# Kernel optimization log

Hardware: AMD Instinct MI355X
Metric: run time of the kernel (lower is better)

## Reference

```python
import jax, jax.numpy as jnp
import numpy as np

N = 50000          # num nodes
E = 800000         # num edges
IN_C = 128         # in_channels
OUT_C = 32         # out_channels
HEADS = 4
R = 8              # num_relations
HC = HEADS * OUT_C # 128
NEG_SLOPE = 0.2


def setup_inputs() -> dict:
    key = jax.random.key(0)
    k1, k2, k3, k4, k5, k6 = jax.random.split(key, 6)
    x = jax.random.normal(k1, (N, IN_C), dtype=jnp.float32)
    edge_index = jax.random.randint(k2, (2, E), 0, N, dtype=jnp.int64)
    edge_type = jax.random.randint(k3, (E,), 0, R, dtype=jnp.int64)
    # glorot init for params
    def glorot(k, shape, fan):
        lim = jnp.sqrt(6.0 / fan)
        return jax.random.uniform(k, shape, jnp.float32, -lim, lim)
    weight = glorot(k4, (R, IN_C, HC), IN_C + HC)       # [R, in, H*C]
    q = glorot(k5, (HC, HEADS), HC + HEADS)             # [H*C, H*dim], dim=1
    kk = glorot(k6, (HC, HEADS), HC + HEADS)
    bias = jnp.zeros((HC,), dtype=jnp.float32)
    return {"x": x, "edge_index": edge_index, "edge_type": edge_type,
            "weight": weight, "q": q, "k": kk, "bias": bias}


def reference(x, edge_index, edge_type, weight, q, k, bias):
    src, dst = edge_index[0], edge_index[1]  # x_j = x[src], x_i = x[dst]
    # Relation-specific transform: precompute per-node per-relation transform
    # (equivalent math to per-edge bmm with index_select'd weights).
    T = jnp.einsum('ni,rio->nro', x, weight)        # [N, R, HC]
    outi = T[dst, edge_type]                        # [E, HC]
    outj = T[src, edge_type]                        # [E, HC]
    qi = outi @ q                                   # [E, H]
    kj = outj @ k                                   # [E, H]
    alpha = jax.nn.leaky_relu(qi + kj, NEG_SLOPE)   # additive-self-attention
    # across-relation softmax over incoming edges of each target node
    amax = jax.ops.segment_max(alpha, dst, num_segments=N)       # [N, H]
    amax = jnp.where(jnp.isfinite(amax), amax, 0.0)
    ex = jnp.exp(alpha - amax[dst])
    denom = jax.ops.segment_sum(ex, dst, num_segments=N)         # [N, H]
    alpha = ex / (denom[dst] + 1e-16)               # [E, H]
    # message (mod=None, dropout=0): outj * alpha, then scatter-add aggregate
    msg = outj.reshape(E, HEADS, OUT_C) * alpha[:, :, None]      # [E, H, C]
    out = jax.ops.segment_sum(msg, dst, num_segments=N)          # [N, H, C]
    return out.reshape(N, HC) + bias                # concat=True
```

## Files before the change

### kernel.cpp

```cpp
#include <hip/hip_runtime.h>

#define NN 50000
#define EE 800000
#define INC 128
#define HCC 128
#define RR 8
#define HH 4
#define CHUNK 256

typedef __attribute__((ext_vector_type(8))) short bf16x8;
typedef __attribute__((ext_vector_type(4))) float f32x4;

static __device__ __forceinline__ unsigned f2b_rne(float f) {
    unsigned u = __float_as_uint(f);
    return (u + 0x7FFFu + ((u >> 16) & 1u)) >> 16;
}
static __device__ __forceinline__ float b2f(unsigned short s) {
    return __uint_as_float(((unsigned)s) << 16);
}


__global__ __launch_bounds__(256) void k_cvt_x(const float* __restrict__ x,
                                               unsigned short* __restrict__ xb) {
    int t = blockIdx.x * 256 + threadIdx.x;
    const float4* p = (const float4*)x + t * 2;
    float4 v0 = p[0], v1 = p[1];
    uint4 pk;
    pk.x = f2b_rne(v0.x) | (f2b_rne(v0.y) << 16);
    pk.y = f2b_rne(v0.z) | (f2b_rne(v0.w) << 16);
    pk.z = f2b_rne(v1.x) | (f2b_rne(v1.y) << 16);
    pk.w = f2b_rne(v1.z) | (f2b_rne(v1.w) << 16);
    *((uint4*)xb + t) = pk;
}

__global__ __launch_bounds__(256) void k_cvt_wt(const float* __restrict__ W,
                                                unsigned short* __restrict__ Wt) {
    int t = blockIdx.x * 256 + threadIdx.x;
    int m = t & 127, kb = (t >> 7) & 15, r = t >> 11;
    unsigned short tmp[8];
#pragma unroll
    for (int j = 0; j < 8; ++j)
        tmp[j] = (unsigned short)f2b_rne(W[((r << 7) + (kb << 3) + j) * 128 + m]);
    uint4 pk;
    pk.x = tmp[0] | ((unsigned)tmp[1] << 16);
    pk.y = tmp[2] | ((unsigned)tmp[3] << 16);
    pk.z = tmp[4] | ((unsigned)tmp[5] << 16);
    pk.w = tmp[6] | ((unsigned)tmp[7] << 16);
    *(uint4*)(Wt + ((r << 7) + m) * 128 + (kb << 3)) = pk;
}

__global__ __launch_bounds__(128) void k_wqk(const float* __restrict__ W,
                                             const float* __restrict__ qw,
                                             const float* __restrict__ kw,
                                             unsigned short* __restrict__ Wqkt) {
    int r = blockIdx.x, i = threadIdx.x;
    const float* wrow = W + (r * INC + i) * HCC;
    float aq0 = 0, aq1 = 0, aq2 = 0, aq3 = 0;
    float ak0 = 0, ak1 = 0, ak2 = 0, ak3 = 0;
    for (int o = 0; o < HCC; ++o) {
        float w = wrow[o];
        float4 qv = *(const float4*)(qw + o * 4);
        float4 kv = *(const float4*)(kw + o * 4);
        aq0 = fmaf(w, qv.x, aq0); aq1 = fmaf(w, qv.y, aq1);
        aq2 = fmaf(w, qv.z, aq2); aq3 = fmaf(w, qv.w, aq3);
        ak0 = fmaf(w, kv.x, ak0); ak1 = fmaf(w, kv.y, ak1);
        ak2 = fmaf(w, kv.z, ak2); ak3 = fmaf(w, kv.w, ak3);
    }
    int cq = r * 4, ck = 32 + r * 4;
    Wqkt[(cq + 0) * 128 + i] = (unsigned short)f2b_rne(aq0);
    Wqkt[(cq + 1) * 128 + i] = (unsigned short)f2b_rne(aq1);
    Wqkt[(cq + 2) * 128 + i] = (unsigned short)f2b_rne(aq2);
    Wqkt[(cq + 3) * 128 + i] = (unsigned short)f2b_rne(aq3);
    Wqkt[(ck + 0) * 128 + i] = (unsigned short)f2b_rne(ak0);
    Wqkt[(ck + 1) * 128 + i] = (unsigned short)f2b_rne(ak1);
    Wqkt[(ck + 2) * 128 + i] = (unsigned short)f2b_rne(ak2);
    Wqkt[(ck + 3) * 128 + i] = (unsigned short)f2b_rne(ak3);
}

__global__ __launch_bounds__(256, 4) void k_qk(const unsigned short* __restrict__ xb,
                                               const unsigned short* __restrict__ Wqkt,
                                               float* __restrict__ QT,
                                               float* __restrict__ KT) {
    int wave = (blockIdx.x * 256 + threadIdx.x) >> 6;
    int lane = threadIdx.x & 63;
    int nt0 = wave * 2, nt1 = nt0 + 1;
    if (nt0 >= 3125) return;
    bool has1 = nt1 < 3125;
    int ln = lane & 15, kq = lane >> 4;

    const unsigned short* x0 = xb + (nt0 * 16 + ln) * 128 + kq * 8;
    const unsigned short* x1 = xb + ((has1 ? nt1 : nt0) * 16 + ln) * 128 + kq * 8;
    bf16x8 b0[4], b1[4];
#pragma unroll
    for (int ks = 0; ks < 4; ++ks) {
        b0[ks] = *(const bf16x8*)(x0 + ks * 32);
        b1[ks] = *(const bf16x8*)(x1 + ks * 32);
    }
    const unsigned short* ab = Wqkt + ln * 128 + kq * 8;
#pragma unroll
    for (int mg = 0; mg < 4; ++mg) {
        f32x4 acc0 = {0.f, 0.f, 0.f, 0.f};
        f32x4 acc1 = {0.f, 0.f, 0.f, 0.f};
#pragma unroll
        for (int ks = 0; ks < 4; ++ks) {
            bf16x8 a = *(const bf16x8*)(ab + mg * 2048 + ks * 32);
            acc0 = __builtin_amdgcn_mfma_f32_16x16x32_bf16(a, b0[ks], acc0, 0, 0, 0);
            acc1 = __builtin_amdgcn_mfma_f32_16x16x32_bf16(a, b1[ks], acc1, 0, 0, 0);
        }
        float* base = (mg < 2) ? QT : KT;
        int rr = (mg & 1) * 4 + kq;
        *(f32x4*)(base + ((nt0 * 16 + ln) * 8 + rr) * 4) = acc0;
        if (has1) *(f32x4*)(base + ((nt1 * 16 + ln) * 8 + rr) * 4) = acc1;
    }
}

__global__ __launch_bounds__(256, 4) void k_T(const unsigned short* __restrict__ xb,
                                              const unsigned short* __restrict__ Wt,
                                              unsigned short* __restrict__ T) {
    int wave = (blockIdx.x * 256 + threadIdx.x) >> 6;
    int lane = threadIdx.x & 63;
    int r = wave & 7;
    int p = wave >> 3;
    int nt0 = p * 2, nt1 = nt0 + 1;
    bool has1 = nt1 < 3125;
    int ln = lane & 15, kq = lane >> 4;

    const unsigned short* x0 = xb + (nt0 * 16 + ln) * 128 + kq * 8;
    const unsigned short* x1 = xb + ((has1 ? nt1 : nt0) * 16 + ln) * 128 + kq * 8;
    bf16x8 b0[4], b1[4];
#pragma unroll
    for (int ks = 0; ks < 4; ++ks) {
        b0[ks] = *(const bf16x8*)(x0 + ks * 32);
        b1[ks] = *(const bf16x8*)(x1 + ks * 32);
    }
    const unsigned short* wb = Wt + (r * 128 + ln) * 128 + kq * 8;
#pragma unroll
    for (int mg2 = 0; mg2 < 4; ++mg2) {
        f32x4 e0 = {0.f, 0.f, 0.f, 0.f};
        f32x4 o0 = {0.f, 0.f, 0.f, 0.f};
        f32x4 e1 = {0.f, 0.f, 0.f, 0.f};
        f32x4 o1 = {0.f, 0.f, 0.f, 0.f};
#pragma unroll
        for (int ks = 0; ks < 4; ++ks) {
            bf16x8 ae = *(const bf16x8*)(wb + (2 * mg2) * 2048 + ks * 32);
            bf16x8 ao = *(const bf16x8*)(wb + (2 * mg2 + 1) * 2048 + ks * 32);
            e0 = __builtin_amdgcn_mfma_f32_16x16x32_bf16(ae, b0[ks], e0, 0, 0, 0);
            o0 = __builtin_amdgcn_mfma_f32_16x16x32_bf16(ao, b0[ks], o0, 0, 0, 0);
            e1 = __builtin_amdgcn_mfma_f32_16x16x32_bf16(ae, b1[ks], e1, 0, 0, 0);
            o1 = __builtin_amdgcn_mfma_f32_16x16x32_bf16(ao, b1[ks], o1, 0, 0, 0);
        }
        uint4 pk0, pk1;
        pk0.x = f2b_rne(e0[0]) | (f2b_rne(e0[1]) << 16);
        pk0.y = f2b_rne(e0[2]) | (f2b_rne(e0[3]) << 16);
        pk0.z = f2b_rne(o0[0]) | (f2b_rne(o0[1]) << 16);
        pk0.w = f2b_rne(o0[2]) | (f2b_rne(o0[3]) << 16);
        pk1.x = f2b_rne(e1[0]) | (f2b_rne(e1[1]) << 16);
        pk1.y = f2b_rne(e1[2]) | (f2b_rne(e1[3]) << 16);
        pk1.z = f2b_rne(o1[0]) | (f2b_rne(o1[1]) << 16);
        pk1.w = f2b_rne(o1[2]) | (f2b_rne(o1[3]) << 16);
        int pos = mg2 * 32 + kq * 8;
        *(uint4*)(T + ((nt0 * 16 + ln) * 8 + r) * 128 + pos) = pk0;
        if (has1) *(uint4*)(T + ((nt1 * 16 + ln) * 8 + r) * 128 + pos) = pk1;
    }
}

__global__ __launch_bounds__(256) void k_hist(const int* __restrict__ ei,
                                              int* __restrict__ deg) {
    int e = blockIdx.x * 256 + threadIdx.x;
    if (e >= EE) return;
    atomicAdd(&deg[ei[EE + e]], 1);
}

__global__ __launch_bounds__(1024) void k_scan1(const int* __restrict__ deg,
                                                int* __restrict__ rowptr,
                                                int* __restrict__ bsum) {
    __shared__ int s[1024];
    int tid = threadIdx.x;
    int g = blockIdx.x * 1024 + tid;
    int v = (g < NN) ? deg[g] : 0;
    s[tid] = v;
    __syncthreads();
    for (int off = 1; off < 1024; off <<= 1) {
        int t = (tid >= off) ? s[tid - off] : 0;
        __syncthreads();
        s[tid] += t;
        __syncthreads();
    }
    if (g < NN) rowptr[g + 1] = s[tid];
    if (tid == 1023) bsum[blockIdx.x] = s[1023];
}

__global__ void k_scan2(const int* __restrict__ bsum, int* __restrict__ boff) {
    int tid = threadIdx.x;
    const int NB = (NN + 1023) / 1024;
    int v = (tid < NB) ? bsum[tid] : 0;
    int orig = v;
    for (int off = 1; off < 64; off <<= 1) {
        int t = __shfl_up(v, off);
        if (tid >= off) v += t;
    }
    if (tid < NB) boff[tid] = v - orig;
}

__global__ __launch_bounds__(1024) void k_scan3(int* __restrict__ rowptr,
                                                const int* __restrict__ boff) {
    int tid = threadIdx.x;
    int g = blockIdx.x * 1024 + tid;
    if (g == 0) rowptr[0] = 0;
    if (g < NN) rowptr[g + 1] += boff[blockIdx.x];
}

__global__ __launch_bounds__(256) void k_scatter(const int* __restrict__ ei,
                                                 const int* __restrict__ et,
                                                 const int* __restrict__ rowptr,
                                                 int* __restrict__ cursor,
                                                 unsigned* __restrict__ srow) {
    int e = blockIdx.x * 256 + threadIdx.x;
    if (e >= EE) return;
    int src = ei[e], dst = ei[EE + e], r = et[e];
    int pos = rowptr[dst] + atomicAdd(&cursor[dst], 1);
    srow[pos] = (unsigned)(src * RR + r);
}

__global__ __launch_bounds__(64) void k_attagg(const int* __restrict__ rowptr,
                                               const unsigned* __restrict__ srow,
                                               const float* __restrict__ QT,
                                               const float* __restrict__ KT,
                                               const unsigned short* __restrict__ T,
                                               const float* __restrict__ bias,
                                               float* __restrict__ out) {
    __shared__ float als[CHUNK * 4];
    __shared__ unsigned srw[CHUNK];
    __shared__ float qs[32];
    const int n = blockIdx.x;
    const int lane = threadIdx.x;
    const int h = lane >> 4;
    const int c = lane * 2;
    const int mgv = c >> 4, kqv = (c >> 2) & 3, regv = c & 3;
    const int posu = (mgv >> 1) * 32 + kqv * 8 + (mgv & 1) * 4 + regv;
    const int beg = rowptr[n], end = rowptr[n + 1];

    if (lane < 32) qs[lane] = QT[n * 32 + lane];
    __syncthreads();

    float m0 = -3.0e38f, m1 = -3.0e38f, m2 = -3.0e38f, m3 = -3.0e38f;
    float d0 = 0.f, d1 = 0.f, d2 = 0.f, d3 = 0.f;
    float accx = 0.f, accy = 0.f;

    for (int j0 = beg; j0 < end; j0 += CHUNK) {
        const int cnt = min(CHUNK, end - j0);
        float lm0 = -3.0e38f, lm1 = -3.0e38f, lm2 = -3.0e38f, lm3 = -3.0e38f;
        for (int jj = lane; jj < cnt; jj += 64) {
            unsigned sr = srow[j0 + jj];
            srw[jj] = sr;
            int r = sr & 7;
            float4 kj = *(const float4*)(KT + sr * 4);
            float a0 = qs[r * 4 + 0] + kj.x;
            float a1 = qs[r * 4 + 1] + kj.y;
            float a2 = qs[r * 4 + 2] + kj.z;
            float a3 = qs[r * 4 + 3] + kj.w;
            a0 = a0 > 0.f ? a0 : 0.2f * a0;
            a1 = a1 > 0.f ? a1 : 0.2f * a1;
            a2 = a2 > 0.f ? a2 : 0.2f * a2;
            a3 = a3 > 0.f ? a3 : 0.2f * a3;
            als[jj * 4 + 0] = a0; als[jj * 4 + 1] = a1;
            als[jj * 4 + 2] = a2; als[jj * 4 + 3] = a3;
            lm0 = fmaxf(lm0, a0); lm1 = fmaxf(lm1, a1);
            lm2 = fmaxf(lm2, a2); lm3 = fmaxf(lm3, a3);
        }
        __syncthreads();
#pragma unroll
        for (int off = 1; off < 64; off <<= 1) {
            lm0 = fmaxf(lm0, __shfl_xor(lm0, off));
            lm1 = fmaxf(lm1, __shfl_xor(lm1, off));
            lm2 = fmaxf(lm2, __shfl_xor(lm2, off));
            lm3 = fmaxf(lm3, __shfl_xor(lm3, off));
        }
        float nm0 = fmaxf(m0, lm0), nm1 = fmaxf(m1, lm1);
        float nm2 = fmaxf(m2, lm2), nm3 = fmaxf(m3, lm3);
        float s0 = expf(m0 - nm0), s1 = expf(m1 - nm1);
        float s2 = expf(m2 - nm2), s3 = expf(m3 - nm3);
        d0 *= s0; d1 *= s1; d2 *= s2; d3 *= s3;
        float sh = h == 0 ? s0 : h == 1 ? s1 : h == 2 ? s2 : s3;
        accx *= sh; accy *= sh;
        m0 = nm0; m1 = nm1; m2 = nm2; m3 = nm3;
        float p0 = 0.f, p1 = 0.f, p2 = 0.f, p3 = 0.f;
        for (int jj = lane; jj < cnt; jj += 64) {
            float e0 = expf(als[jj * 4 + 0] - m0);
            float e1 = expf(als[jj * 4 + 1] - m1);
            float e2 = expf(als[jj * 4 + 2] - m2);
            float e3 = expf(als[jj * 4 + 3] - m3);
            als[jj * 4 + 0] = e0; als[jj * 4 + 1] = e1;
            als[jj * 4 + 2] = e2; als[jj * 4 + 3] = e3;
            p0 += e0; p1 += e1; p2 += e2; p3 += e3;
        }
#pragma unroll
        for (int off = 1; off < 64; off <<= 1) {
            p0 += __shfl_xor(p0, off);
            p1 += __shfl_xor(p1, off);
            p2 += __shfl_xor(p2, off);
            p3 += __shfl_xor(p3, off);
        }
        d0 += p0; d1 += p1; d2 += p2; d3 += p3;
        __syncthreads();
        for (int jj = 0; jj < cnt; ++jj) {
            float w = als[jj * 4 + h];
            unsigned pk = *(const unsigned*)(T + srw[jj] * 128 + posu);
            accx = fmaf(w, b2f((unsigned short)(pk & 0xFFFF)), accx);
            accy = fmaf(w, b2f((unsigned short)(pk >> 16)), accy);
        }
        __syncthreads();
    }
    float dh = h == 0 ? d0 : h == 1 ? d1 : h == 2 ? d2 : d3;
    float inv = 1.f / (dh + 1e-16f);
    out[n * 128 + c] = accx * inv + bias[c];
    out[n * 128 + c + 1] = accy * inv + bias[c + 1];
}

extern "C" void kernel_launch(void* const* d_in, const int* in_sizes, int n_in,
                              void* d_out, int out_size, void* d_ws, size_t ws_size,
                              hipStream_t stream) {
    const float* x    = (const float*)d_in[0];
    const int*   ei   = (const int*)d_in[1];
    const int*   et   = (const int*)d_in[2];
    const float* W    = (const float*)d_in[3];
    const float* qw   = (const float*)d_in[4];
    const float* kw   = (const float*)d_in[5];
    const float* bias = (const float*)d_in[6];
    float* out = (float*)d_out;
    char* ws = (char*)d_ws;

    unsigned short* T    = (unsigned short*)(ws + 0);
    float* QT            = (float*)(ws + 102400000);
    float* KT            = (float*)(ws + 108800000);
    unsigned short* Wqkt = (unsigned short*)(ws + 115200000);
    int* deg             = (int*)(ws + 115220480);
    int* cursor          = (int*)(ws + 115420480);
    int* rowptr          = (int*)(ws + 115620480);
    int* bsum            = (int*)(ws + 115820484);
    int* boff            = (int*)(ws + 115820740);
    unsigned* srow       = (unsigned*)(ws + 115820996);
    unsigned short* xb   = (unsigned short*)(ws + 119021056);
    unsigned short* Wt   = (unsigned short*)(ws + 131821056);

    hipMemsetAsync(ws + 115220480, 0, 400000, stream);

    k_cvt_x<<<3125, 256, 0, stream>>>(x, xb);
    k_cvt_wt<<<64, 256, 0, stream>>>(W, Wt);
    k_wqk<<<RR, 128, 0, stream>>>(W, qw, kw, Wqkt);
    k_qk<<<391, 256, 0, stream>>>(xb, Wqkt, QT, KT);
    k_T<<<3126, 256, 0, stream>>>(xb, Wt, T);
    k_hist<<<(EE + 255) / 256, 256, 0, stream>>>(ei, deg);
    k_scan1<<<49, 1024, 0, stream>>>(deg, rowptr, bsum);
    k_scan2<<<1, 64, 0, stream>>>(bsum, boff);
    k_scan3<<<49, 1024, 0, stream>>>(rowptr, boff);
    k_scatter<<<(EE + 255) / 256, 256, 0, stream>>>(ei, et, rowptr, cursor, srow);
    k_attagg<<<NN, 64, 0, stream>>>(rowptr, srow, QT, KT, T, bias, out);
}
```

Baseline: 311.3 us.

## Stage per-relation weights in XOR-swizzled LDS for the node-transform GEMM

Each k_T block now loads one relation's 128x128 bf16 weight tile into shared memory, stored in an XOR-swizzled layout that k_cvt_wt writes, and then computes 16 node tiles against it. The MFMA A operands are read from LDS instead of from global memory once per wave. This cuts global/L2 weight traffic and spreads LDS reads across banks. In exchange it needs a 32KB LDS allocation and a block barrier, drops the occupancy hint, and launches fewer, larger blocks.

```diff
diff --git a/kernel.cpp b/kernel.cpp
--- a/kernel.cpp
+++ b/kernel.cpp
@@ -34,7 +34,7 @@
 }
 
 __global__ __launch_bounds__(256) void k_cvt_wt(const float* __restrict__ W,
-                                                unsigned short* __restrict__ Wt) {
+                                                unsigned short* __restrict__ Wts) {
     int t = blockIdx.x * 256 + threadIdx.x;
     int m = t & 127, kb = (t >> 7) & 15, r = t >> 11;
     unsigned short tmp[8];
@@ -46,7 +46,8 @@
     pk.y = tmp[2] | ((unsigned)tmp[3] << 16);
     pk.z = tmp[4] | ((unsigned)tmp[5] << 16);
     pk.w = tmp[6] | ((unsigned)tmp[7] << 16);
-    *(uint4*)(Wt + ((r << 7) + m) * 128 + (kb << 3)) = pk;
+    int idx = r * 2048 + m * 16 + (kb ^ (m & 15));
+    *((uint4*)Wts + idx) = pk;
 }
 
 __global__ __launch_bounds__(128) void k_wqk(const float* __restrict__ W,
@@ -114,53 +115,69 @@
     }
 }
 
-__global__ __launch_bounds__(256, 4) void k_T(const unsigned short* __restrict__ xb,
-                                              const unsigned short* __restrict__ Wt,
-                                              unsigned short* __restrict__ T) {
-    int wave = (blockIdx.x * 256 + threadIdx.x) >> 6;
-    int lane = threadIdx.x & 63;
-    int r = wave & 7;
-    int p = wave >> 3;
-    int nt0 = p * 2, nt1 = nt0 + 1;
-    bool has1 = nt1 < 3125;
-    int ln = lane & 15, kq = lane >> 4;
-
-    const unsigned short* x0 = xb + (nt0 * 16 + ln) * 128 + kq * 8;
-    const unsigned short* x1 = xb + ((has1 ? nt1 : nt0) * 16 + ln) * 128 + kq * 8;
-    bf16x8 b0[4], b1[4];
-#pragma unroll
-    for (int ks = 0; ks < 4; ++ks) {
-        b0[ks] = *(const bf16x8*)(x0 + ks * 32);
-        b1[ks] = *(const bf16x8*)(x1 + ks * 32);
-    }
-    const unsigned short* wb = Wt + (r * 128 + ln) * 128 + kq * 8;
-#pragma unroll
-    for (int mg2 = 0; mg2 < 4; ++mg2) {
-        f32x4 e0 = {0.f, 0.f, 0.f, 0.f};
-        f32x4 o0 = {0.f, 0.f, 0.f, 0.f};
-        f32x4 e1 = {0.f, 0.f, 0.f, 0.f};
-        f32x4 o1 = {0.f, 0.f, 0.f, 0.f};
+__global__ __launch_bounds__(256) void k_T(const unsigned short* __restrict__ xb,
+                                           const unsigned short* __restrict__ Wts,
+                                           unsigned short* __restrict__ T) {
+    __shared__ unsigned short lA[16384];
+    const int r = blockIdx.x & 7;
+    const int grp = blockIdx.x >> 3;
+    const int tid = threadIdx.x;
+    const int wv = tid >> 6, lane = tid & 63;
+    const int ln = lane & 15, kq = lane >> 4;
+
+    {
+        const uint4* src = (const uint4*)Wts + r * 2048;
+        uint4* dst = (uint4*)lA;
+#pragma unroll
+        for (int i = 0; i < 8; ++i) dst[i * 256 + tid] = src[i * 256 + tid];
+    }
+    __syncthreads();
+
+#pragma unroll
+    for (int g = 0; g < 2; ++g) {
+        int nt0 = grp * 16 + g * 8 + wv * 2;
+        int nt1 = nt0 + 1;
+        bool h0 = nt0 < 3125, h1 = nt1 < 3125;
+        int a0 = h0 ? nt0 : 3124, a1 = h1 ? nt1 : 3124;
+        const unsigned short* x0 = xb + (a0 * 16 + ln) * 128 + kq * 8;
+        const unsigned short* x1 = xb + (a1 * 16 + ln) * 128 + kq * 8;
+        bf16x8 b0[4], b1[4];
 #pragma unroll
         for (int ks = 0; ks < 4; ++ks) {
-            bf16x8 ae = *(const bf16x8*)(wb + (2 * mg2) * 2048 + ks * 32);
-            bf16x8 ao = *(const bf16x8*)(wb + (2 * mg2 + 1) * 2048 + ks * 32);
-            e0 = __builtin_amdgcn_mfma_f32_16x16x32_bf16(ae, b0[ks], e0, 0, 0, 0);
-            o0 = __builtin_amdgcn_mfma_f32_16x16x32_bf16(ao, b0[ks], o0, 0, 0, 0);
-            e1 = __builtin_amdgcn_mfma_f32_16x16x32_bf16(ae, b1[ks], e1, 0, 0, 0);
-            o1 = __builtin_amdgcn_mfma_f32_16x16x32_bf16(ao, b1[ks], o1, 0, 0, 0);
-        }
-        uint4 pk0, pk1;
-        pk0.x = f2b_rne(e0[0]) | (f2b_rne(e0[1]) << 16);
-        pk0.y = f2b_rne(e0[2]) | (f2b_rne(e0[3]) << 16);
-        pk0.z = f2b_rne(o0[0]) | (f2b_rne(o0[1]) << 16);
-        pk0.w = f2b_rne(o0[2]) | (f2b_rne(o0[3]) << 16);
-        pk1.x = f2b_rne(e1[0]) | (f2b_rne(e1[1]) << 16);
-        pk1.y = f2b_rne(e1[2]) | (f2b_rne(e1[3]) << 16);
-        pk1.z = f2b_rne(o1[0]) | (f2b_rne(o1[1]) << 16);
-        pk1.w = f2b_rne(o1[2]) | (f2b_rne(o1[3]) << 16);
-        int pos = mg2 * 32 + kq * 8;
-        *(uint4*)(T + ((nt0 * 16 + ln) * 8 + r) * 128 + pos) = pk0;
-        if (has1) *(uint4*)(T + ((nt1 * 16 + ln) * 8 + r) * 128 + pos) = pk1;
+            b0[ks] = *(const bf16x8*)(x0 + ks * 32);
+            b1[ks] = *(const bf16x8*)(x1 + ks * 32);
+        }
+#pragma unroll
+        for (int mg2 = 0; mg2 < 4; ++mg2) {
+            f32x4 e0 = {0.f, 0.f, 0.f, 0.f};
+            f32x4 o0 = {0.f, 0.f, 0.f, 0.f};
+            f32x4 e1 = {0.f, 0.f, 0.f, 0.f};
+            f32x4 o1 = {0.f, 0.f, 0.f, 0.f};
+            const int rowe = mg2 * 32 + ln;
+            const int rowo = mg2 * 32 + 16 + ln;
+#pragma unroll
+            for (int ks = 0; ks < 4; ++ks) {
+                int ch = (kq + ks * 4) ^ ln;
+                bf16x8 ae = *(const bf16x8*)(lA + rowe * 128 + ch * 8);
+                bf16x8 ao = *(const bf16x8*)(lA + rowo * 128 + ch * 8);
+                e0 = __builtin_amdgcn_mfma_f32_16x16x32_bf16(ae, b0[ks], e0, 0, 0, 0);
+                o0 = __builtin_amdgcn_mfma_f32_16x16x32_bf16(ao, b0[ks], o0, 0, 0, 0);
+                e1 = __builtin_amdgcn_mfma_f32_16x16x32_bf16(ae, b1[ks], e1, 0, 0, 0);
+                o1 = __builtin_amdgcn_mfma_f32_16x16x32_bf16(ao, b1[ks], o1, 0, 0, 0);
+            }
+            uint4 pk0, pk1;
+            pk0.x = f2b_rne(e0[0]) | (f2b_rne(e0[1]) << 16);
+            pk0.y = f2b_rne(e0[2]) | (f2b_rne(e0[3]) << 16);
+            pk0.z = f2b_rne(o0[0]) | (f2b_rne(o0[1]) << 16);
+            pk0.w = f2b_rne(o0[2]) | (f2b_rne(o0[3]) << 16);
+            pk1.x = f2b_rne(e1[0]) | (f2b_rne(e1[1]) << 16);
+            pk1.y = f2b_rne(e1[2]) | (f2b_rne(e1[3]) << 16);
+            pk1.z = f2b_rne(o1[0]) | (f2b_rne(o1[1]) << 16);
+            pk1.w = f2b_rne(o1[2]) | (f2b_rne(o1[3]) << 16);
+            int pos = mg2 * 32 + kq * 8;
+            if (h0) *(uint4*)(T + ((nt0 * 16 + ln) * 8 + r) * 128 + pos) = pk0;
+            if (h1) *(uint4*)(T + ((nt1 * 16 + ln) * 8 + r) * 128 + pos) = pk1;
+        }
     }
 }
 
@@ -341,15 +358,15 @@
     int* boff            = (int*)(ws + 115820740);
     unsigned* srow       = (unsigned*)(ws + 115820996);
     unsigned short* xb   = (unsigned short*)(ws + 119021056);
-    unsigned short* Wt   = (unsigned short*)(ws + 131821056);
+    unsigned short* Wts  = (unsigned short*)(ws + 131821056);
 
     hipMemsetAsync(ws + 115220480, 0, 400000, stream);
 
     k_cvt_x<<<3125, 256, 0, stream>>>(x, xb);
-    k_cvt_wt<<<64, 256, 0, stream>>>(W, Wt);
+    k_cvt_wt<<<64, 256, 0, stream>>>(W, Wts);
     k_wqk<<<RR, 128, 0, stream>>>(W, qw, kw, Wqkt);
     k_qk<<<391, 256, 0, stream>>>(xb, Wqkt, QT, KT);
-    k_T<<<3126, 256, 0, stream>>>(xb, Wt, T);
+    k_T<<<8 * 196, 256, 0, stream>>>(xb, Wts, T);
     k_hist<<<(EE + 255) / 256, 256, 0, stream>>>(ei, deg);
     k_scan1<<<49, 1024, 0, stream>>>(deg, rowptr, bsum);
     k_scan2<<<1, 64, 0, stream>>>(bsum, boff);
```

New measurement: 280.2 us. 10.0% less time.
